# Optimization experiments

Measured on AMD Instinct MI355X. Metric: run time of the kernel, lower is better.

The kernel has to match this reference:

```python
import jax, jax.numpy as jnp
import numpy as np

H = 16  # num_heads
THETA = 10000.0


def _rope(x, position):
    # x: (B, H, N, hd), position: (B, N) float
    B, h, N, hd = x.shape
    freqs = 1.0 / (THETA ** (jnp.arange(0, hd, 2, dtype=jnp.float32) / hd))  # (hd/2,)
    ang = position[:, None, :, None] * freqs  # (B, 1, N, hd/2)
    cos, sin = jnp.cos(ang), jnp.sin(ang)
    xr = x.reshape(B, h, N, hd // 2, 2)
    re, im = xr[..., 0], xr[..., 1]
    out_re = re * cos - im * sin
    out_im = re * sin + im * cos
    return jnp.stack([out_re, out_im], axis=-1).reshape(B, h, N, hd)


def setup_inputs() -> dict:
    key = jax.random.key(0)
    ks = jax.random.split(key, 6)
    B, N, D = 4, 2049, 1024
    x = jax.random.normal(ks[0], (B, N, D), dtype=jnp.float32)
    position = jnp.sort(jax.random.randint(ks[1], (B, N - 1), 0, 8192), axis=-1).astype(jnp.int32)
    w_qkv = jax.random.normal(ks[2], (3 * D, D), dtype=jnp.float32) * (1.0 / np.sqrt(D))
    b_qkv = jax.random.normal(ks[3], (3 * D,), dtype=jnp.float32) * 0.02
    w_fc = jax.random.normal(ks[4], (D, D), dtype=jnp.float32) * (1.0 / np.sqrt(D))
    b_fc = jax.random.normal(ks[5], (D,), dtype=jnp.float32) * 0.02
    return {"x": x, "position": position, "w_qkv": w_qkv, "b_qkv": b_qkv, "w_fc": w_fc, "b_fc": b_fc}


def reference(x, position, w_qkv, b_qkv, w_fc, b_fc):
    B, N, D = x.shape
    hd = D // H
    # fused QKV projection
    qkv = x @ w_qkv.T + b_qkv                      # (B, N, 3D)
    qkv = qkv.reshape(B, N, 3, H, hd)
    qkv = jnp.transpose(qkv, (2, 0, 3, 1, 4))       # (3, B, H, N, hd)
    q, k, v = qkv[0], qkv[1], qkv[2]
    # rotary on non-cls tokens, cls passthrough
    pos_f = position.astype(jnp.float32)
    q = jnp.concatenate([q[:, :, :1, :], _rope(q[:, :, 1:, :], pos_f)], axis=2)
    k = jnp.concatenate([k[:, :, :1, :], _rope(k[:, :, 1:, :], pos_f)], axis=2)
    # SDPA (no causal mask, eval mode -> no dropout)
    scale = 1.0 / jnp.sqrt(jnp.float32(hd))
    scores = jnp.einsum('bhqd,bhkd->bhqk', q, k) * scale
    attn = jax.nn.softmax(scores, axis=-1)
    out = jnp.einsum('bhqk,bhkd->bhqd', attn, v)    # (B, H, N, hd)
    out = jnp.transpose(out, (0, 2, 1, 3)).reshape(B, N, D)
    out = out @ w_fc.T + b_fc
    return out
```

## Files before the change

### kernel.cpp

```cpp
#include <hip/hip_runtime.h>

typedef unsigned short u16;
typedef __attribute__((ext_vector_type(8))) _Float16 f16x8;
typedef __attribute__((ext_vector_type(4))) float f32x4;

#define MFMAH(a, b, c) __builtin_amdgcn_mfma_f32_16x16x32_f16((a), (b), (c), 0, 0, 0)

__device__ __forceinline__ u16 f2h(float f) {
  _Float16 h = (_Float16)f;
  return __builtin_bit_cast(u16, h);
}
__device__ __forceinline__ float h2f(u16 h) {
  return (float)__builtin_bit_cast(_Float16, h);
}
__device__ __forceinline__ unsigned pk_h(float a, float b) {
  return (unsigned)f2h(a) | ((unsigned)f2h(b) << 16);
}
__device__ __forceinline__ unsigned pkrtz(float a, float b) {
  unsigned r;
  asm("v_cvt_pkrtz_f16_f32 %0, %1, %2" : "=v"(r) : "v"(a), "v"(b));
  return r;
}

__global__ void prep_cast(const float* __restrict__ x, u16* __restrict__ xh,
                          const float* __restrict__ wqf, u16* __restrict__ wq,
                          const float* __restrict__ wff, u16* __restrict__ wf,
                          long nx, long nq, long nf) {
  long total = nx + nq + nf;
  long stride = (long)gridDim.x * blockDim.x;
  for (long i = (long)blockIdx.x * blockDim.x + threadIdx.x; i < total; i += stride) {
    const float4* src;
    ushort4* dst;
    long j;
    if (i < nx) { src = (const float4*)x; dst = (ushort4*)xh; j = i; }
    else if (i < nx + nq) { src = (const float4*)wqf; dst = (ushort4*)wq; j = i - nx; }
    else { src = (const float4*)wff; dst = (ushort4*)wf; j = i - nx - nq; }
    float4 v = src[j];
    ushort4 h;
    h.x = f2h(v.x); h.y = f2h(v.y); h.z = f2h(v.z); h.w = f2h(v.w);
    dst[j] = h;
  }
}

__global__ void cs_table_kernel(const int* __restrict__ pos, float2* __restrict__ cst) {
  int idx = blockIdx.x * 256 + threadIdx.x;
  int i = idx & 31;
  int r = idx >> 5;
  int ti = r & 2047;
  int b = r >> 11;
  int p = pos[b * 2048 + ti];
  float fr = (float)pow(10000.0, -(double)i / 32.0);
  float angf = (float)p * fr;
  double sd, cd;
  sincos((double)angf, &sd, &cd);
  cst[idx] = make_float2((float)cd, (float)sd);
}

__global__ void kpad_kernel(u16* __restrict__ kh, int N, int NP) {
  const int per_bh = (NP - N) * 32;
  int idx = blockIdx.x * 256 + threadIdx.x;
  if (idx >= 64 * per_bh) return;
  int bh = idx / per_bh, r = idx - bh * per_bh;
  size_t u = (((size_t)bh * NP + N) * 64 >> 1) + r;
  ((unsigned*)kh)[u] = 0;
}

__global__ __launch_bounds__(256) void vtransT_kernel(const u16* __restrict__ vb_,
                                                      u16* __restrict__ ot, int N, int NP) {
  __shared__ u16 tile[64][72];
  const int bh = blockIdx.y;
  const int t0 = blockIdx.x * 64;
  const u16* ih = vb_ + (size_t)bh * N * 64;
#pragma unroll
  for (int p = 0; p < 4; ++p) {
    int idx = p * 256 + threadIdx.x;
    int tloc = idx >> 4, c = (idx & 15) * 4;
    int t = t0 + tloc;
    ushort4 a = make_ushort4(0, 0, 0, 0);
    if (t < N) a = *(const ushort4*)(ih + (size_t)t * 64 + c);
    *(ushort4*)&tile[tloc][c] = a;
  }
  __syncthreads();
  u16* oh = ot + (size_t)bh * 64 * NP;
#pragma unroll
  for (int p = 0; p < 4; ++p) {
    int idx = p * 256 + threadIdx.x;
    int d = idx >> 4, tq = (idx & 15) * 4;
    int t = t0 + tq;
    if (t < NP) {
      ushort4 a;
      a.x = tile[tq + 0][d]; a.y = tile[tq + 1][d];
      a.z = tile[tq + 2][d]; a.w = tile[tq + 3][d];
      *(ushort4*)(oh + (size_t)d * NP + t) = a;
    }
  }
}

__device__ __forceinline__ int swz_off(int R, int lg) {
  return R * 32 + ((lg ^ ((R >> 1) & 3)) << 3);
}
__device__ __forceinline__ void stage_tile(const u16* __restrict__ g, u16* l,
                                           int row0, int rmax, int K, int k0, int tid) {
#pragma unroll
  for (int t = 0; t < 2; ++t) {
    int c = t * 256 + tid;
    int row = c >> 2;
    int kc = (((c & 3) ^ ((c >> 3) & 3)) << 3);
    int gr = row0 + row;
    if (gr > rmax) gr = rmax;
    const u16* gp = g + (size_t)gr * K + (k0 + kc);
    __builtin_amdgcn_global_load_lds((const __attribute__((address_space(1))) void*)gp,
                                     (__attribute__((address_space(3))) void*)(l + c * 8),
                                     16, 0, 0);
  }
}

template <int EPI>
__global__ __launch_bounds__(256) void gemm_s1(
    const u16* __restrict__ Aw, const u16* __restrict__ Bw,
    const float* __restrict__ bias, const float2* __restrict__ cst,
    float* __restrict__ outf,
    u16* __restrict__ oq, u16* __restrict__ ok, u16* __restrict__ ov,
    int M, int Nn, int K, int Ntok, int NP) {
  __shared__ u16 A0[4096], B0[4096], A1[4096], B1[4096];
  const int tid = threadIdx.x;
  const int wid = tid >> 6, lane = tid & 63;
  const int wm = wid >> 1, wn = wid & 1;
  const int lg = lane >> 4, lm = lane & 15;
  const int id = blockIdx.x;
  const int chunk = (int)gridDim.x >> 3, nx = Nn >> 7;
  const int swz = (id & 7) * chunk + (id >> 3);
  const int mbase = (swz / nx) * 128, nbase = (swz % nx) * 128;

  f32x4 acc[4][4];
  const f32x4 zero = {0.f, 0.f, 0.f, 0.f};
#pragma unroll
  for (int a = 0; a < 4; ++a)
#pragma unroll
    for (int b = 0; b < 4; ++b) acc[a][b] = zero;

  stage_tile(Aw, A0, mbase, M - 1, K, 0, tid);
  stage_tile(Bw, B0, nbase, Nn - 1, K, 0, tid);
  __syncthreads();

  for (int k0 = 0; k0 < K; k0 += 64) {
    if (k0 + 32 < K) {
      stage_tile(Aw, A1, mbase, M - 1, K, k0 + 32, tid);
      stage_tile(Bw, B1, nbase, Nn - 1, K, k0 + 32, tid);
    }
    {
      f16x8 a[4], w[4];
#pragma unroll
      for (int f = 0; f < 4; ++f) {
        a[f] = *(const f16x8*)&A0[swz_off(wm * 64 + f * 16 + lm, lg)];
        w[f] = *(const f16x8*)&B0[swz_off(wn * 64 + f * 16 + lm, lg)];
      }
#pragma unroll
      for (int fm = 0; fm < 4; ++fm)
#pragma unroll
        for (int fn = 0; fn < 4; ++fn) acc[fm][fn] = MFMAH(a[fm], w[fn], acc[fm][fn]);
    }
    __syncthreads();
    if (k0 + 64 < K) {
      stage_tile(Aw, A0, mbase, M - 1, K, k0 + 64, tid);
      stage_tile(Bw, B0, nbase, Nn - 1, K, k0 + 64, tid);
    }
    {
      f16x8 a[4], w[4];
#pragma unroll
      for (int f = 0; f < 4; ++f) {
        a[f] = *(const f16x8*)&A1[swz_off(wm * 64 + f * 16 + lm, lg)];
        w[f] = *(const f16x8*)&B1[swz_off(wn * 64 + f * 16 + lm, lg)];
      }
#pragma unroll
      for (int fm = 0; fm < 4; ++fm)
#pragma unroll
        for (int fn = 0; fn < 4; ++fn) acc[fm][fn] = MFMAH(a[fm], w[fn], acc[fm][fn]);
    }
    __syncthreads();
  }

  const int which = (EPI == 0) ? (nbase >> 10) : 1;
  const bool odd = (lm & 1);
#pragma unroll
  for (int fm = 0; fm < 4; ++fm)
#pragma unroll
    for (int fn = 0; fn < 4; ++fn) {
      int col = nbase + wn * 64 + fn * 16 + lm;
      float bv = bias[col];
      int h2 = (col >> 6) & 15, d2 = col & 63;
#pragma unroll
      for (int i = 0; i < 4; ++i) {
        int row = mbase + wm * 64 + fm * 16 + lg * 4 + i;
        float v = acc[fm][fn][i] + bv;
        float partner = __shfl_xor(v, 1);
        if (row < M) {
          if (EPI == 1) {
            outf[(size_t)row * Nn + col] = v;
          } else {
            int b2 = row / Ntok, t2 = row - b2 * Ntok;
            int bh2 = b2 * 16 + h2;
            if (which == 2) {
              ov[((size_t)bh2 * Ntok + t2) * 64 + d2] = f2h(v);
            } else {
              float out = v;
              if (t2 > 0) {
                float2 cs = cst[((size_t)(b2 << 11) + (t2 - 1)) * 32 + (d2 >> 1)];
                out = v * cs.x + (odd ? partner * cs.y : -partner * cs.y);
              }
              if (which == 0) {
                out *= 0.18033688011112042f;
                oq[((size_t)bh2 * Ntok + t2) * 64 + d2] = f2h(out);
              } else {
                ok[((size_t)bh2 * NP + t2) * 64 + d2] = f2h(out);
              }
            }
          }
        }
      }
    }
}

template <bool DO_STAGE, bool TAIL>
__device__ __forceinline__ void attn_tile(
    int kv0, int kvn,
    const u16* Kc, const u16* Vc, u16* Kn, u16* Vn,
    const u16* kgb, const u16* vgb,
    int tid, int lg, int lm, int kvbase,
    const f16x8 (&qf16)[2][2],
    float (&m_)[2], float (&l_)[2], f32x4 (&oacc)[2][4],
    unsigned (*pexw)[64][4], int N) {
  if (DO_STAGE) {
    __builtin_amdgcn_global_load_lds(
        (const __attribute__((address_space(1))) void*)(kgb + (size_t)kvn * 64),
        (__attribute__((address_space(3))) void*)(Kn + tid * 8), 16, 0, 0);
    __builtin_amdgcn_global_load_lds(
        (const __attribute__((address_space(1))) void*)(vgb + kvn),
        (__attribute__((address_space(3))) void*)(Vn + tid * 8), 16, 0, 0);
  }

  const f32x4 zero = {0.f, 0.f, 0.f, 0.f};
  f32x4 s[2][4];
#pragma unroll
  for (int qf = 0; qf < 2; ++qf)
#pragma unroll
    for (int cf = 0; cf < 4; ++cf) s[qf][cf] = zero;
#pragma unroll
  for (int cf = 0; cf < 4; ++cf)
#pragma unroll
    for (int dk = 0; dk < 2; ++dk) {
      f16x8 kf = *(const f16x8*)&Kc[kvbase + dk * 2048 + cf * 128];
      s[0][cf] = MFMAH(kf, qf16[0][dk], s[0][cf]);
      s[1][cf] = MFMAH(kf, qf16[1][dk], s[1][cf]);
    }
  if (TAIL) {
#pragma unroll
    for (int qf = 0; qf < 2; ++qf)
#pragma unroll
      for (int cf = 0; cf < 4; ++cf)
#pragma unroll
        for (int i = 0; i < 4; ++i)
          if (kv0 + cf * 16 + lg * 4 + i >= N) s[qf][cf][i] = -1e30f;
  }

  unsigned us[2][8];
#pragma unroll
  for (int qf = 0; qf < 2; ++qf) {
    float t0 = fmaxf(fmaxf(s[qf][0][0], s[qf][0][1]), fmaxf(s[qf][0][2], s[qf][0][3]));
    float t1 = fmaxf(fmaxf(s[qf][1][0], s[qf][1][1]), fmaxf(s[qf][1][2], s[qf][1][3]));
    float t2 = fmaxf(fmaxf(s[qf][2][0], s[qf][2][1]), fmaxf(s[qf][2][2], s[qf][2][3]));
    float t3 = fmaxf(fmaxf(s[qf][3][0], s[qf][3][1]), fmaxf(s[qf][3][2], s[qf][3][3]));
    float mx = fmaxf(fmaxf(t0, t1), fmaxf(t2, t3));
    float mr = m_[qf];
    bool nore = __all(mx - mr <= 8.f) != 0;
    float mnew = mr;
    if (!nore) {
      float rmx = fmaxf(mx, __shfl_xor(mx, 16));
      rmx = fmaxf(rmx, __shfl_xor(rmx, 32));
      mnew = fmaxf(mr, rmx);
    }
    float p[16];
#pragma unroll
    for (int cf = 0; cf < 4; ++cf)
#pragma unroll
      for (int i = 0; i < 4; ++i)
        p[cf * 4 + i] = __builtin_amdgcn_exp2f(s[qf][cf][i] - mnew);
    float ps = 0.f;
#pragma unroll
    for (int j = 0; j < 16; ++j) ps += p[j];
    if (nore) {
      l_[qf] += ps;
    } else {
      float sc = __builtin_amdgcn_exp2f(mr - mnew);
      l_[qf] = l_[qf] * sc + ps;
      m_[qf] = mnew;
#pragma unroll
      for (int c = 0; c < 4; ++c)
#pragma unroll
        for (int i = 0; i < 4; ++i) oacc[qf][c][i] *= sc;
    }
#pragma unroll
    for (int w = 0; w < 8; ++w) us[qf][w] = pkrtz(p[2 * w], p[2 * w + 1]);
  }

  f16x8 pb[2][2];
  const int ga = (lg & 1) * 2, gb = ga + 1;
  const int cfs2 = (lg >> 1) * 2;
  const int prow = lg * 16 + lm;
#pragma unroll
  for (int ks = 0; ks < 2; ++ks) {
    *(uint4*)&pexw[0][prow][0] =
        make_uint4(us[0][ks * 4], us[0][ks * 4 + 1], us[0][ks * 4 + 2], us[0][ks * 4 + 3]);
    *(uint4*)&pexw[1][prow][0] =
        make_uint4(us[1][ks * 4], us[1][ks * 4 + 1], us[1][ks * 4 + 2], us[1][ks * 4 + 3]);
#pragma unroll
    for (int qf = 0; qf < 2; ++qf) {
      uint2 r0 = *(const uint2*)&pexw[qf][ga * 16 + lm][cfs2];
      uint2 r1 = *(const uint2*)&pexw[qf][gb * 16 + lm][cfs2];
      uint4 pu = make_uint4(r0.x, r0.y, r1.x, r1.y);
      pb[qf][ks] = __builtin_bit_cast(f16x8, pu);
    }
  }

#pragma unroll
  for (int c = 0; c < 4; ++c)
#pragma unroll
    for (int ks = 0; ks < 2; ++ks) {
      f16x8 vh = *(const f16x8*)&Vc[kvbase + ks * 2048 + c * 128];
      oacc[0][c] = MFMAH(vh, pb[0][ks], oacc[0][c]);
      oacc[1][c] = MFMAH(vh, pb[1][ks], oacc[1][c]);
    }
}

__global__ __launch_bounds__(512, 4) void attn_kernel(
    const u16* __restrict__ qh, const u16* __restrict__ kh, const u16* __restrict__ vth,
    u16* __restrict__ outh, int N, int NP) {
  __shared__ u16 K0[4096], V0[4096], K1[4096], V1[4096];
  __shared__ unsigned pexm[8][2][64][4];

  const int id = blockIdx.x;
  const int swz = (id & 7) * 72 + (id >> 3);
  const int qblk = swz % 9;
  const int bh = swz / 9;
  const int b = bh >> 4, h = bh & 15;
  const int tid = threadIdx.x;
  const int wid = tid >> 6, lane = tid & 63;
  const int lg = lane >> 4, lm = lane & 15;
  const int qbase = qblk * 256 + wid * 32;
  const size_t qoff = (size_t)bh * N * 64;
  const size_t koff = (size_t)bh * NP * 64;
  const size_t voff = (size_t)bh * 64 * NP;

  const int jK = tid & 63, rK = tid >> 6;
  const u16* kgb = kh + koff + (size_t)jK * 64 + rK * 8;
  const u16* vgb = vth + voff + (size_t)jK * NP + rK * 8;
  const int kvbase = lg * 512 + lm * 8;

  f16x8 qf16[2][2];
#pragma unroll
  for (int qf = 0; qf < 2; ++qf) {
    int qr = qbase + qf * 16 + lm;
    if (qr > N - 1) qr = N - 1;
    const u16* qp = qh + qoff + (size_t)qr * 64 + lg * 8;
    qf16[qf][0] = *(const f16x8*)(qp);
    qf16[qf][1] = *(const f16x8*)(qp + 32);
  }

  const f32x4 zero = {0.f, 0.f, 0.f, 0.f};
  f32x4 oacc[2][4];
#pragma unroll
  for (int qf = 0; qf < 2; ++qf)
#pragma unroll
    for (int c = 0; c < 4; ++c) oacc[qf][c] = zero;
  float m_[2] = {-1e30f, -1e30f}, l_[2] = {0.f, 0.f};
  unsigned(*pexw)[64][4] = pexm[wid];

  __builtin_amdgcn_global_load_lds(
      (const __attribute__((address_space(1))) void*)kgb,
      (__attribute__((address_space(3))) void*)(K0 + tid * 8), 16, 0, 0);
  __builtin_amdgcn_global_load_lds(
      (const __attribute__((address_space(1))) void*)vgb,
      (__attribute__((address_space(3))) void*)(V0 + tid * 8), 16, 0, 0);
  asm volatile("s_waitcnt vmcnt(0)" ::: "memory");
  __builtin_amdgcn_s_barrier();

  for (int t = 0; t < 32; t += 2) {
    attn_tile<true, false>(t * 64, (t + 1) * 64, K0, V0, K1, V1, kgb, vgb,
                           tid, lg, lm, kvbase, qf16, m_, l_, oacc, pexw, N);
    asm volatile("s_waitcnt vmcnt(0)" ::: "memory");
    __builtin_amdgcn_s_barrier();
    attn_tile<true, false>((t + 1) * 64, (t + 2) * 64, K1, V1, K0, V0, kgb, vgb,
                           tid, lg, lm, kvbase, qf16, m_, l_, oacc, pexw, N);
    asm volatile("s_waitcnt vmcnt(0)" ::: "memory");
    __builtin_amdgcn_s_barrier();
  }
  attn_tile<false, true>(32 * 64, 0, K0, V0, K1, V1, kgb, vgb,
                         tid, lg, lm, kvbase, qf16, m_, l_, oacc, pexw, N);

#pragma unroll
  for (int qf = 0; qf < 2; ++qf) {
    int t = qbase + qf * 16 + lm;
    float lt = l_[qf];
    lt += __shfl_xor(lt, 16);
    lt += __shfl_xor(lt, 32);
    if (t < N) {
      float rl = 1.f / lt;
      size_t rowoff = ((size_t)(b * N + t)) * 1024 + h * 64 + lg * 4;
#pragma unroll
      for (int c = 0; c < 4; ++c) {
        float v0 = oacc[qf][c][0] * rl, v1 = oacc[qf][c][1] * rl;
        float v2 = oacc[qf][c][2] * rl, v3 = oacc[qf][c][3] * rl;
        unsigned hh01 = pk_h(v0, v1), hh23 = pk_h(v2, v3);
        *(uint2*)(outh + rowoff + c * 16) = make_uint2(hh01, hh23);
      }
    }
  }
}

extern "C" void kernel_launch(void* const* d_in, const int* in_sizes, int n_in,
                              void* d_out, int out_size, void* d_ws, size_t ws_size,
                              hipStream_t stream) {
  const float* x     = (const float*)d_in[0];
  const int*   pos   = (const int*)  d_in[1];
  const float* w_qkv = (const float*)d_in[2];
  const float* b_qkv = (const float*)d_in[3];
  const float* w_fc  = (const float*)d_in[4];
  const float* b_fc  = (const float*)d_in[5];
  (void)in_sizes; (void)n_in; (void)out_size; (void)ws_size;

  const int B = 4, N = 2049, NP = 2112;
  const long EL = (long)B * N * 1024;
  const long ELP = (long)B * 16 * NP * 64;

  char* base = (char*)d_ws;
  size_t off = 0;
  auto alloc = [&](size_t bytes) -> void* {
    void* p = base + off;
    off += (bytes + 255) & ~(size_t)255;
    return p;
  };
  u16* qhh = (u16*)alloc(EL * 2);
  u16* khh = (u16*)alloc(ELP * 2);
  u16* vbh = (u16*)alloc(EL * 2);
  u16* vth = (u16*)alloc((size_t)64 * 64 * NP * 2);
  u16* xh  = (u16*)alloc(EL * 2);
  u16* wq  = (u16*)alloc((size_t)3072 * 1024 * 2);
  u16* wf  = (u16*)alloc((size_t)1024 * 1024 * 2);
  float2* cst = (float2*)alloc((size_t)B * 2048 * 32 * 8);

  prep_cast<<<2048, 256, 0, stream>>>(x, xh, w_qkv, wq, w_fc, wf,
                                      EL / 4, (long)3072 * 1024 / 4, (long)1024 * 1024 / 4);
  cs_table_kernel<<<(B * 2048 * 32) / 256, 256, 0, stream>>>(pos, cst);
  gemm_s1<0><<<dim3(1560), 256, 0, stream>>>(xh, wq, b_qkv, cst, nullptr,
                                             qhh, khh, vbh, 8196, 3072, 1024, N, NP);
  kpad_kernel<<<(64 * (NP - N) * 32 + 255) / 256, 256, 0, stream>>>(khh, N, NP);
  vtransT_kernel<<<dim3(NP / 64, 64), 256, 0, stream>>>(vbh, vth, N, NP);
  attn_kernel<<<dim3(576), 512, 0, stream>>>(qhh, khh, vth, xh, N, NP);
  gemm_s1<1><<<dim3(520), 256, 0, stream>>>(xh, wf, b_fc, nullptr,
                                            (float*)d_out, nullptr, nullptr, nullptr,
                                            8196, 1024, 1024, N, NP);
}
```

Measured before the change: 322.0 us.

## Triple-buffer GEMM LDS tiles with partial vmcnt waits to keep loads in flight

The QKV and output-projection GEMM moves from a double buffer with full __syncthreads to a three-slot LDS ring. Each tile is prefetched two steps ahead. Each step waits only until the older load group has landed (s_waitcnt vmcnt(4)) and then issues one raw barrier, so global loads overlap more with MFMA work. This uses 50% more shared memory, which may lower occupancy. It also depends on each stage issuing exactly the assumed number of loads, which makes the vmcnt accounting fragile.

```diff
diff --git a/kernel.cpp b/kernel.cpp
--- a/kernel.cpp
+++ b/kernel.cpp
@@ -122,7 +122,7 @@
     float* __restrict__ outf,
     u16* __restrict__ oq, u16* __restrict__ ok, u16* __restrict__ ov,
     int M, int Nn, int K, int Ntok, int NP) {
-  __shared__ u16 A0[4096], B0[4096], A1[4096], B1[4096];
+  __shared__ u16 Ab[3][4096], Bb[3][4096];
   const int tid = threadIdx.x;
   const int wid = tid >> 6, lane = tid & 63;
   const int wm = wid >> 1, wn = wid & 1;
@@ -139,45 +139,43 @@
 #pragma unroll
     for (int b = 0; b < 4; ++b) acc[a][b] = zero;
 
-  stage_tile(Aw, A0, mbase, M - 1, K, 0, tid);
-  stage_tile(Bw, B0, nbase, Nn - 1, K, 0, tid);
-  __syncthreads();
-
-  for (int k0 = 0; k0 < K; k0 += 64) {
-    if (k0 + 32 < K) {
-      stage_tile(Aw, A1, mbase, M - 1, K, k0 + 32, tid);
-      stage_tile(Bw, B1, nbase, Nn - 1, K, k0 + 32, tid);
+  stage_tile(Aw, Ab[0], mbase, M - 1, K, 0, tid);
+  stage_tile(Bw, Bb[0], nbase, Nn - 1, K, 0, tid);
+  stage_tile(Aw, Ab[1], mbase, M - 1, K, 32, tid);
+  stage_tile(Bw, Bb[1], nbase, Nn - 1, K, 32, tid);
+  asm volatile("s_waitcnt vmcnt(4)" ::: "memory");
+  asm volatile("s_barrier" ::: "memory");
+
+  const int T = K >> 5;
+  int cur = 0;
+  for (int t = 0; t < T; ++t) {
+    int nxt = cur + 2; if (nxt >= 3) nxt -= 3;
+    if (t + 2 < T) {
+      stage_tile(Aw, Ab[nxt], mbase, M - 1, K, (t + 2) << 5, tid);
+      stage_tile(Bw, Bb[nxt], nbase, Nn - 1, K, (t + 2) << 5, tid);
     }
     {
+      const u16* cA = Ab[cur];
+      const u16* cB = Bb[cur];
       f16x8 a[4], w[4];
 #pragma unroll
       for (int f = 0; f < 4; ++f) {
-        a[f] = *(const f16x8*)&A0[swz_off(wm * 64 + f * 16 + lm, lg)];
-        w[f] = *(const f16x8*)&B0[swz_off(wn * 64 + f * 16 + lm, lg)];
+        a[f] = *(const f16x8*)&cA[swz_off(wm * 64 + f * 16 + lm, lg)];
+        w[f] = *(const f16x8*)&cB[swz_off(wn * 64 + f * 16 + lm, lg)];
       }
 #pragma unroll
       for (int fm = 0; fm < 4; ++fm)
 #pragma unroll
         for (int fn = 0; fn < 4; ++fn) acc[fm][fn] = MFMAH(a[fm], w[fn], acc[fm][fn]);
     }
-    __syncthreads();
-    if (k0 + 64 < K) {
-      stage_tile(Aw, A0, mbase, M - 1, K, k0 + 64, tid);
-      stage_tile(Bw, B0, nbase, Nn - 1, K, k0 + 64, tid);
-    }
-    {
-      f16x8 a[4], w[4];
-#pragma unroll
-      for (int f = 0; f < 4; ++f) {
-        a[f] = *(const f16x8*)&A1[swz_off(wm * 64 + f * 16 + lm, lg)];
-        w[f] = *(const f16x8*)&B1[swz_off(wn * 64 + f * 16 + lm, lg)];
-      }
-#pragma unroll
-      for (int fm = 0; fm < 4; ++fm)
-#pragma unroll
-        for (int fn = 0; fn < 4; ++fn) acc[fm][fn] = MFMAH(a[fm], w[fn], acc[fm][fn]);
-    }
-    __syncthreads();
+    if (t < T - 2) {
+      asm volatile("s_waitcnt vmcnt(4)" ::: "memory");
+      asm volatile("s_barrier" ::: "memory");
+    } else if (t == T - 2) {
+      asm volatile("s_waitcnt vmcnt(0)" ::: "memory");
+      asm volatile("s_barrier" ::: "memory");
+    }
+    cur = cur + 1; if (cur >= 3) cur = 0;
   }
 
   const int which = (EPI == 0) ? (nbase >> 10) : 1;
```

New measurement: 344.3 us. 1.07x slower.
